# Optimization experiments

Hardware: AMD Instinct MI355X
Metric: run time of the kernel (lower is better)

The kernel has to match this reference:

```python
import jax, jax.numpy as jnp
import numpy as np

D = 1024  # input_size == hidden_size
T = 8192  # decoder sequence length


def setup_inputs() -> dict:
    key = jax.random.key(0)
    ks = jax.random.split(key, 12)
    s = 1.0 / np.sqrt(2 * D)  # nn.Linear default init scale
    return {
        "target_seq": jax.random.normal(ks[0], (T, D), dtype=jnp.float32),
        "encoder_h": jax.random.normal(ks[1], (D,), dtype=jnp.float32),
        "encoder_c": jax.random.normal(ks[2], (D,), dtype=jnp.float32),
        "W_f": jax.random.normal(ks[3], (D, 2 * D), dtype=jnp.float32) * s,
        "b_f": jax.random.normal(ks[4], (D,), dtype=jnp.float32) * 0.1,
        "W_i": jax.random.normal(ks[5], (D, 2 * D), dtype=jnp.float32) * s,
        "b_i": jax.random.normal(ks[6], (D,), dtype=jnp.float32) * 0.1,
        "W_C": jax.random.normal(ks[7], (D, 2 * D), dtype=jnp.float32) * s,
        "b_C": jax.random.normal(ks[8], (D,), dtype=jnp.float32) * 0.1,
        "W_o": jax.random.normal(ks[9], (D, 2 * D), dtype=jnp.float32) * s,
        "b_o": jax.random.normal(ks[10], (D,), dtype=jnp.float32) * 0.1,
        "tf": 0,
    }


def reference(target_seq, encoder_h, encoder_c, W_f, b_f, W_i, b_i, W_C, b_C, W_o, b_o, tf):
    # tf_ratio is hard-coded 0.0 in the source, so teacher forcing never fires.
    def step(carry, x_t):
        h, c = carry
        z_hx = jnp.concatenate([h, x_t])   # cat([h_{t-1}, x_t])
        z_hc = jnp.concatenate([h, c])     # quirk: Ctilde gets cat([h_{t-1}, c_{t-1}])
        f = jax.nn.sigmoid(W_f @ z_hx + b_f)
        i = jax.nn.sigmoid(W_i @ z_hx + b_i)
        ctilde = jnp.tanh(W_C @ z_hc + b_C)
        c_new = f * c + i * ctilde
        o = jax.nn.sigmoid(W_o @ z_hx + b_o)
        h_new = o * jnp.tanh(c_new)
        return (h_new, c_new), h_new

    (_, _), predictions = jax.lax.scan(step, (encoder_h, encoder_c), target_seq)
    return predictions  # [T, D]
```

## Files before the change

kernel.cpp:

```cpp
#include <hip/hip_runtime.h>

#define DD 1024
#define TT 8192
#define NBLK 128
#define NTHR 512
#define RPB 8
#define WLDS (RPB * 4 * DD)
#define LDSB (WLDS * 4 + DD * 8)

__device__ __forceinline__ float fast_sigmoid(float x) {
  x = fminf(fmaxf(x, -30.0f), 30.0f);
  return 1.0f / (1.0f + __expf(-x));
}

__device__ __forceinline__ float fast_tanh(float x) {
  x = fminf(fmaxf(x, -15.0f), 15.0f);
  float e = __expf(2.0f * x);
  return (e - 1.0f) / (e + 1.0f);
}

union HC { unsigned long long u; float2 f; };

__global__ __launch_bounds__(NTHR, 2) void lstm_seq(
    const float* __restrict__ X,
    const float* __restrict__ enc_h,
    const float* __restrict__ enc_c,
    const float* __restrict__ Wf, const float* __restrict__ bf_,
    const float* __restrict__ Wi, const float* __restrict__ bi_,
    const float* __restrict__ Wc, const float* __restrict__ bc_,
    const float* __restrict__ Wo, const float* __restrict__ bo_,
    float* __restrict__ out,
    unsigned long long* __restrict__ hcbuf,
    unsigned* __restrict__ flags)
{
  extern __shared__ float lds[];
  const int wv   = threadIdx.x >> 6;
  const int lane = threadIdx.x & 63;
  const int j    = blockIdx.x * RPB + wv;

  for (int idx = threadIdx.x; idx < RPB * 4 * 256; idx += NTHR) {
    const int r = idx >> 10, g = (idx >> 8) & 3, q = idx & 255;
    const int row = blockIdx.x * RPB + r;
    const float* ws = (g == 0) ? Wf : (g == 1) ? Wi : (g == 2) ? Wo : Wc;
    *(float4*)&lds[idx * 4] = *(const float4*)(ws + (size_t)row * 2048 + q * 4);
  }

  float wxf[16], wxi[16], wxo[16], wcc[16];
#pragma unroll
  for (int kb = 0; kb < 4; ++kb) {
    const int k = 1024 + kb * 256 + lane * 4;
    *(float4*)&wxf[kb*4] = *(const float4*)(Wf + (size_t)j * 2048 + k);
    *(float4*)&wxi[kb*4] = *(const float4*)(Wi + (size_t)j * 2048 + k);
    *(float4*)&wxo[kb*4] = *(const float4*)(Wo + (size_t)j * 2048 + k);
    *(float4*)&wcc[kb*4] = *(const float4*)(Wc + (size_t)j * 2048 + k);
  }
  const float Bf = bf_[j], Bi = bi_[j], Bc = bc_[j], Bo = bo_[j];
  const float* lw = lds + wv * 4096;
  float* hsh = lds + WLDS;
  float* hsc = lds + WLDS + DD;

  float cj = enc_c[j];

  __syncthreads();

  float4 xc0, xc1, xc2, xc3;
  {
    const float* xq = X + lane * 4;
    xc0 = *(const float4*)(xq);       xc1 = *(const float4*)(xq + 256);
    xc2 = *(const float4*)(xq + 512); xc3 = *(const float4*)(xq + 768);
  }

  for (int t = 0; t < TT; ++t) {
    float4 xn0, xn1, xn2, xn3;
    {
      const size_t tn = (t + 1 < TT) ? (size_t)(t + 1) : (size_t)t;
      const float* xq = X + tn * DD + lane * 4;
      xn0 = *(const float4*)(xq);       xn1 = *(const float4*)(xq + 256);
      xn2 = *(const float4*)(xq + 512); xn3 = *(const float4*)(xq + 768);
    }

    float aF = 0.0f, aI = 0.0f, aO = 0.0f, aC = 0.0f;
#pragma unroll
    for (int kb = 0; kb < 4; ++kb) {
      const float4 xv = (kb==0)?xc0:(kb==1)?xc1:(kb==2)?xc2:xc3;
      const int b = kb * 4;
      aF += wxf[b]*xv.x + wxf[b+1]*xv.y + wxf[b+2]*xv.z + wxf[b+3]*xv.w;
      aI += wxi[b]*xv.x + wxi[b+1]*xv.y + wxi[b+2]*xv.z + wxi[b+3]*xv.w;
      aO += wxo[b]*xv.x + wxo[b+1]*xv.y + wxo[b+2]*xv.z + wxo[b+3]*xv.w;
    }

    if (t > 0) {
      if (wv < 2) {
        const unsigned tt = (unsigned)t;
        const int half = wv;
        for (;;) {
          unsigned a = __hip_atomic_load(&flags[half * 64 + lane],
                                         __ATOMIC_RELAXED, __HIP_MEMORY_SCOPE_AGENT);
          if (__all(a >= tt)) break;
        }
        const unsigned long long* src =
            hcbuf + (size_t)((t - 1) & 1) * DD + half * 512 + lane * 4;
        unsigned long long raw[8];
#pragma unroll
        for (int kb = 0; kb < 2; ++kb) {
#pragma unroll
          for (int q = 0; q < 4; ++q) {
            raw[kb*4+q] = __hip_atomic_load(src + kb * 256 + q,
                                            __ATOMIC_RELAXED, __HIP_MEMORY_SCOPE_AGENT);
          }
        }
#pragma unroll
        for (int kb = 0; kb < 2; ++kb) {
          const int o = half * 512 + kb * 256 + lane * 4;
          HC u0, u1, u2, u3;
          u0.u = raw[kb*4+0]; u1.u = raw[kb*4+1];
          u2.u = raw[kb*4+2]; u3.u = raw[kb*4+3];
          *(float4*)&hsh[o] = make_float4(u0.f.x, u1.f.x, u2.f.x, u3.f.x);
          *(float4*)&hsc[o] = make_float4(u0.f.y, u1.f.y, u2.f.y, u3.f.y);
        }
      }
      __syncthreads();
    }

    if (t == 0) {
      const float* hp = enc_h + lane * 4;
      const float* cp = enc_c + lane * 4;
#pragma unroll
      for (int kb = 0; kb < 4; ++kb) {
        const int o = kb * 256 + lane * 4;
        const float4 hv = *(const float4*)(hp + kb * 256);
        const float4 cc = *(const float4*)(cp + kb * 256);
        const float4 wF = *(const float4*)&lw[o];
        const float4 wI = *(const float4*)&lw[1024 + o];
        const float4 wO = *(const float4*)&lw[2048 + o];
        const float4 wC = *(const float4*)&lw[3072 + o];
        const int b = kb * 4;
        aF += wF.x*hv.x + wF.y*hv.y + wF.z*hv.z + wF.w*hv.w;
        aI += wI.x*hv.x + wI.y*hv.y + wI.z*hv.z + wI.w*hv.w;
        aO += wO.x*hv.x + wO.y*hv.y + wO.z*hv.z + wO.w*hv.w;
        aC += wC.x*hv.x + wC.y*hv.y + wC.z*hv.z + wC.w*hv.w;
        aC += wcc[b]*cc.x + wcc[b+1]*cc.y + wcc[b+2]*cc.z + wcc[b+3]*cc.w;
      }
    } else {
#pragma unroll
      for (int kb = 0; kb < 4; ++kb) {
        const int o = kb * 256 + lane * 4;
        const float4 hv = *(const float4*)&hsh[o];
        const float4 cc = *(const float4*)&hsc[o];
        const float4 wF = *(const float4*)&lw[o];
        const float4 wI = *(const float4*)&lw[1024 + o];
        const float4 wO = *(const float4*)&lw[2048 + o];
        const float4 wC = *(const float4*)&lw[3072 + o];
        const int b = kb * 4;
        aF += wF.x*hv.x + wF.y*hv.y + wF.z*hv.z + wF.w*hv.w;
        aI += wI.x*hv.x + wI.y*hv.y + wI.z*hv.z + wI.w*hv.w;
        aO += wO.x*hv.x + wO.y*hv.y + wO.z*hv.z + wO.w*hv.w;
        aC += wC.x*hv.x + wC.y*hv.y + wC.z*hv.z + wC.w*hv.w;
        aC += wcc[b]*cc.x + wcc[b+1]*cc.y + wcc[b+2]*cc.z + wcc[b+3]*cc.w;
      }
    }

#pragma unroll
    for (int m = 32; m >= 1; m >>= 1) {
      aF += __shfl_xor(aF, m, 64);
      aI += __shfl_xor(aI, m, 64);
      aO += __shfl_xor(aO, m, 64);
      aC += __shfl_xor(aC, m, 64);
    }

    const float fg = fast_sigmoid(aF + Bf);
    const float ig = fast_sigmoid(aI + Bi);
    const float og = fast_sigmoid(aO + Bo);
    const float ct = fast_tanh(aC + Bc);
    const float cn = fg * cj + ig * ct;
    const float hn = og * fast_tanh(cn);
    cj = cn;

    if (lane == 0) {
      out[(size_t)t * DD + j] = hn;
      HC u; u.f = make_float2(hn, cn);
      __hip_atomic_store(hcbuf + (size_t)(t & 1) * DD + j, u.u,
                         __ATOMIC_RELAXED, __HIP_MEMORY_SCOPE_AGENT);
    }
    __syncthreads();
    if (threadIdx.x == 0) {
      __hip_atomic_store(&flags[blockIdx.x], (unsigned)(t + 1),
                         __ATOMIC_RELAXED, __HIP_MEMORY_SCOPE_AGENT);
    }
    xc0 = xn0; xc1 = xn1; xc2 = xn2; xc3 = xn3;
  }
}

extern "C" void kernel_launch(void* const* d_in, const int* in_sizes, int n_in,
                              void* d_out, int out_size, void* d_ws, size_t ws_size,
                              hipStream_t stream) {
  const float* X    = (const float*)d_in[0];
  const float* eh   = (const float*)d_in[1];
  const float* ec   = (const float*)d_in[2];
  const float* Wf   = (const float*)d_in[3];
  const float* bf_  = (const float*)d_in[4];
  const float* Wi   = (const float*)d_in[5];
  const float* bi_  = (const float*)d_in[6];
  const float* Wc   = (const float*)d_in[7];
  const float* bc_  = (const float*)d_in[8];
  const float* Wo   = (const float*)d_in[9];
  const float* bo_  = (const float*)d_in[10];
  float* out = (float*)d_out;

  unsigned* flags = (unsigned*)d_ws;
  unsigned long long* hcbuf = (unsigned long long*)((char*)d_ws + 1024);

  hipMemsetAsync(d_ws, 0, 1024, stream);

  hipFuncSetAttribute((const void*)lstm_seq,
                      hipFuncAttributeMaxDynamicSharedMemorySize, LDSB);

  void* args[] = {(void*)&X, (void*)&eh, (void*)&ec,
                  (void*)&Wf, (void*)&bf_, (void*)&Wi, (void*)&bi_,
                  (void*)&Wc, (void*)&bc_, (void*)&Wo, (void*)&bo_,
                  (void*)&out, (void*)&hcbuf, (void*)&flags};
  hipError_t e = hipLaunchCooperativeKernel((const void*)lstm_seq,
                                            dim3(NBLK), dim3(NTHR),
                                            args, LDSB, stream);
  if (e != hipSuccess) {
    lstm_seq<<<dim3(NBLK), dim3(NTHR), LDSB, stream>>>(
        X, eh, ec, Wf, bf_, Wi, bi_, Wc, bc_, Wo, bo_, out, hcbuf, flags);
  }
}
```

Baseline: 28.80 ms.

## Replace per-block flag barrier with step-tagged h/c words polled directly

Drops the separate per-block flag array and end-of-step __syncthreads/flag store. Each published h and c value is now a 64-bit word holding the step number as a tag, and every wave spins on the words it needs. All eight waves gather h and c in parallel, instead of two waves reading flags and then data. This removes one block barrier and one extra global round trip per step, while doubling LDS staging and the number of atomic stores per row. Launch bounds change to one block per CU.

After: 31.75 ms. 10.2% more time.

```diff
diff --git a/kernel.cpp b/kernel.cpp
--- a/kernel.cpp
+++ b/kernel.cpp
@@ -6,7 +6,9 @@
 #define NTHR 512
 #define RPB 8
 #define WLDS (RPB * 4 * DD)
-#define LDSB (WLDS * 4 + DD * 8)
+#define LDSB ((WLDS + 4 * DD) * 4)
+
+typedef unsigned long long u64;
 
 __device__ __forceinline__ float fast_sigmoid(float x) {
   x = fminf(fmaxf(x, -30.0f), 30.0f);
@@ -19,9 +21,11 @@
   return (e - 1.0f) / (e + 1.0f);
 }
 
-union HC { unsigned long long u; float2 f; };
-
-__global__ __launch_bounds__(NTHR, 2) void lstm_seq(
+__device__ __forceinline__ u64 ld_cp(const u64* p) {
+  return __hip_atomic_load(p, __ATOMIC_RELAXED, __HIP_MEMORY_SCOPE_AGENT);
+}
+
+__global__ __launch_bounds__(NTHR, 1) void lstm_seq(
     const float* __restrict__ X,
     const float* __restrict__ enc_h,
     const float* __restrict__ enc_c,
@@ -30,8 +34,8 @@
     const float* __restrict__ Wc, const float* __restrict__ bc_,
     const float* __restrict__ Wo, const float* __restrict__ bo_,
     float* __restrict__ out,
-    unsigned long long* __restrict__ hcbuf,
-    unsigned* __restrict__ flags)
+    u64* __restrict__ hw,
+    u64* __restrict__ cw)
 {
   extern __shared__ float lds[];
   const int wv   = threadIdx.x >> 6;
@@ -56,8 +60,8 @@
   }
   const float Bf = bf_[j], Bi = bi_[j], Bc = bc_[j], Bo = bo_[j];
   const float* lw = lds + wv * 4096;
-  float* hsh = lds + WLDS;
-  float* hsc = lds + WLDS + DD;
+  float* hst = lds + WLDS;
+  float* cst = lds + WLDS + 2 * DD;
 
   float cj = enc_c[j];
 
@@ -90,39 +94,40 @@
     }
 
     if (t > 0) {
-      if (wv < 2) {
-        const unsigned tt = (unsigned)t;
-        const int half = wv;
-        for (;;) {
-          unsigned a = __hip_atomic_load(&flags[half * 64 + lane],
-                                         __ATOMIC_RELAXED, __HIP_MEMORY_SCOPE_AGENT);
-          if (__all(a >= tt)) break;
-        }
-        const unsigned long long* src =
-            hcbuf + (size_t)((t - 1) & 1) * DD + half * 512 + lane * 4;
-        unsigned long long raw[8];
-#pragma unroll
-        for (int kb = 0; kb < 2; ++kb) {
-#pragma unroll
-          for (int q = 0; q < 4; ++q) {
-            raw[kb*4+q] = __hip_atomic_load(src + kb * 256 + q,
-                                            __ATOMIC_RELAXED, __HIP_MEMORY_SCOPE_AGENT);
-          }
-        }
-#pragma unroll
-        for (int kb = 0; kb < 2; ++kb) {
-          const int o = half * 512 + kb * 256 + lane * 4;
-          HC u0, u1, u2, u3;
-          u0.u = raw[kb*4+0]; u1.u = raw[kb*4+1];
-          u2.u = raw[kb*4+2]; u3.u = raw[kb*4+3];
-          *(float4*)&hsh[o] = make_float4(u0.f.x, u1.f.x, u2.f.x, u3.f.x);
-          *(float4*)&hsc[o] = make_float4(u0.f.y, u1.f.y, u2.f.y, u3.f.y);
-        }
+      const unsigned want = (unsigned)t;
+      const int rp = (t - 1) & 1;
+      const u64* src = (wv < 4 ? hw : cw) +
+                       (size_t)rp * DD + (wv & 3) * 256 + lane * 4;
+      float* dst = (wv < 4 ? hst : cst) + rp * DD + (wv & 3) * 256 + lane * 4;
+      u64 w0 = ld_cp(src + 0), w1 = ld_cp(src + 1);
+      u64 w2 = ld_cp(src + 2), w3 = ld_cp(src + 3);
+      while ((unsigned)(w0 >> 32) < want) w0 = ld_cp(src + 0);
+      while ((unsigned)(w1 >> 32) < want) w1 = ld_cp(src + 1);
+      while ((unsigned)(w2 >> 32) < want) w2 = ld_cp(src + 2);
+      while ((unsigned)(w3 >> 32) < want) w3 = ld_cp(src + 3);
+      *(float4*)dst = make_float4(__uint_as_float((unsigned)w0),
+                                  __uint_as_float((unsigned)w1),
+                                  __uint_as_float((unsigned)w2),
+                                  __uint_as_float((unsigned)w3));
+      __syncthreads();
+
+#pragma unroll
+      for (int kb = 0; kb < 4; ++kb) {
+        const int o = kb * 256 + lane * 4;
+        const float4 hv = *(const float4*)&hst[rp * DD + o];
+        const float4 cc = *(const float4*)&cst[rp * DD + o];
+        const float4 wF = *(const float4*)&lw[o];
+        const float4 wI = *(const float4*)&lw[1024 + o];
+        const float4 wO = *(const float4*)&lw[2048 + o];
+        const float4 wC = *(const float4*)&lw[3072 + o];
+        const int b = kb * 4;
+        aF += wF.x*hv.x + wF.y*hv.y + wF.z*hv.z + wF.w*hv.w;
+        aI += wI.x*hv.x + wI.y*hv.y + wI.z*hv.z + wI.w*hv.w;
+        aO += wO.x*hv.x + wO.y*hv.y + wO.z*hv.z + wO.w*hv.w;
+        aC += wC.x*hv.x + wC.y*hv.y + wC.z*hv.z + wC.w*hv.w;
+        aC += wcc[b]*cc.x + wcc[b+1]*cc.y + wcc[b+2]*cc.z + wcc[b+3]*cc.w;
       }
-      __syncthreads();
-    }
-
-    if (t == 0) {
+    } else {
       const float* hp = enc_h + lane * 4;
       const float* cp = enc_c + lane * 4;
 #pragma unroll
@@ -141,23 +146,6 @@
         aC += wC.x*hv.x + wC.y*hv.y + wC.z*hv.z + wC.w*hv.w;
         aC += wcc[b]*cc.x + wcc[b+1]*cc.y + wcc[b+2]*cc.z + wcc[b+3]*cc.w;
       }
-    } else {
-#pragma unroll
-      for (int kb = 0; kb < 4; ++kb) {
-        const int o = kb * 256 + lane * 4;
-        const float4 hv = *(const float4*)&hsh[o];
-        const float4 cc = *(const float4*)&hsc[o];
-        const float4 wF = *(const float4*)&lw[o];
-        const float4 wI = *(const float4*)&lw[1024 + o];
-        const float4 wO = *(const float4*)&lw[2048 + o];
-        const float4 wC = *(const float4*)&lw[3072 + o];
-        const int b = kb * 4;
-        aF += wF.x*hv.x + wF.y*hv.y + wF.z*hv.z + wF.w*hv.w;
-        aI += wI.x*hv.x + wI.y*hv.y + wI.z*hv.z + wI.w*hv.w;
-        aO += wO.x*hv.x + wO.y*hv.y + wO.z*hv.z + wO.w*hv.w;
-        aC += wC.x*hv.x + wC.y*hv.y + wC.z*hv.z + wC.w*hv.w;
-        aC += wcc[b]*cc.x + wcc[b+1]*cc.y + wcc[b+2]*cc.z + wcc[b+3]*cc.w;
-      }
     }
 
 #pragma unroll
@@ -178,13 +166,12 @@
 
     if (lane == 0) {
       out[(size_t)t * DD + j] = hn;
-      HC u; u.f = make_float2(hn, cn);
-      __hip_atomic_store(hcbuf + (size_t)(t & 1) * DD + j, u.u,
+      const u64 tag = ((u64)(unsigned)(t + 1)) << 32;
+      __hip_atomic_store(&hw[(size_t)(t & 1) * DD + j],
+                         tag | (u64)__float_as_uint(hn),
                          __ATOMIC_RELAXED, __HIP_MEMORY_SCOPE_AGENT);
-    }
-    __syncthreads();
-    if (threadIdx.x == 0) {
-      __hip_atomic_store(&flags[blockIdx.x], (unsigned)(t + 1),
+      __hip_atomic_store(&cw[(size_t)(t & 1) * DD + j],
+                         tag | (u64)__float_as_uint(cn),
                          __ATOMIC_RELAXED, __HIP_MEMORY_SCOPE_AGENT);
     }
     xc0 = xn0; xc1 = xn1; xc2 = xn2; xc3 = xn3;
@@ -207,10 +194,10 @@
   const float* bo_  = (const float*)d_in[10];
   float* out = (float*)d_out;
 
-  unsigned* flags = (unsigned*)d_ws;
-  unsigned long long* hcbuf = (unsigned long long*)((char*)d_ws + 1024);
-
-  hipMemsetAsync(d_ws, 0, 1024, stream);
+  u64* hw = (u64*)d_ws;
+  u64* cw = (u64*)((char*)d_ws + 16384);
+
+  hipMemsetAsync(d_ws, 0, 32768, stream);
 
   hipFuncSetAttribute((const void*)lstm_seq,
                       hipFuncAttributeMaxDynamicSharedMemorySize, LDSB);
@@ -218,12 +205,12 @@
   void* args[] = {(void*)&X, (void*)&eh, (void*)&ec,
                   (void*)&Wf, (void*)&bf_, (void*)&Wi, (void*)&bi_,
                   (void*)&Wc, (void*)&bc_, (void*)&Wo, (void*)&bo_,
-                  (void*)&out, (void*)&hcbuf, (void*)&flags};
+                  (void*)&out, (void*)&hw, (void*)&cw};
   hipError_t e = hipLaunchCooperativeKernel((const void*)lstm_seq,
                                             dim3(NBLK), dim3(NTHR),
                                             args, LDSB, stream);
   if (e != hipSuccess) {
     lstm_seq<<<dim3(NBLK), dim3(NTHR), LDSB, stream>>>(
-        X, eh, ec, Wf, bf_, Wi, bi_, Wc, bc_, Wo, bo_, out, hcbuf, flags);
-  }
-}
+        X, eh, ec, Wf, bf_, Wi, bi_, Wc, bc_, Wo, bo_, out, hw, cw);
+  }
+}
```
